# Kernel tuning notes

Measured on AMD Instinct MI355X. Metric: run time of the kernel, lower is better.

## Reference

```python
import jax, jax.numpy as jnp
import numpy as np

LN_EPS = 1e-5


def setup_inputs() -> dict:
    key = jax.random.key(0)
    k1, k2, k3 = jax.random.split(key, 3)
    N, E, D_IN, D_OUT = 50000, 500000, 128, 128
    x = jax.random.normal(k1, (N, D_IN), dtype=jnp.float32)
    edge_index = jax.random.randint(k2, (2, E), 0, N, dtype=jnp.int64)
    W = jax.random.normal(k3, (D_IN, D_OUT), dtype=jnp.float32) * (1.0 / np.sqrt(D_IN))
    b = jnp.zeros((D_OUT,), dtype=jnp.float32)
    ln_gamma = jnp.ones((D_OUT,), dtype=jnp.float32)
    ln_beta = jnp.zeros((D_OUT,), dtype=jnp.float32)
    return {"x": x, "edge_index": edge_index, "W": W, "b": b,
            "ln_gamma": ln_gamma, "ln_beta": ln_beta}


def reference(x, edge_index, W, b, ln_gamma, ln_beta):
    N = x.shape[0]
    # GCNConv: linear transform first (no fused bias; bias added after aggregation)
    h = x @ W  # [N, D_out]
    # add self-loops
    loops = jnp.arange(N, dtype=edge_index.dtype)
    src = jnp.concatenate([edge_index[0], loops])  # [E+N]
    dst = jnp.concatenate([edge_index[1], loops])  # [E+N]
    # symmetric normalization deg^{-1/2} (degree computed on dst, incl. self-loops)
    deg = jax.ops.segment_sum(jnp.ones(src.shape, dtype=h.dtype), dst, num_segments=N)
    dinv = jnp.where(deg > 0, jax.lax.rsqrt(deg), 0.0)
    norm = dinv[src] * dinv[dst]  # [E+N]
    # gather messages, scale, scatter-add to destinations
    msgs = h[src] * norm[:, None]  # [E+N, D_out]
    out = jax.ops.segment_sum(msgs, dst, num_segments=N) + b  # [N, D_out]
    # LayerNorm over features
    mu = out.mean(axis=-1, keepdims=True)
    var = out.var(axis=-1, keepdims=True)
    out = (out - mu) * jax.lax.rsqrt(var + LN_EPS) * ln_gamma + ln_beta
    # activation
    return jax.nn.relu(out)
```

## Files before the change

kernel.cpp:

```cpp
#include <hip/hip_runtime.h>
#include <math.h>

#define D 128
#define LN_EPS 1e-5f
#define BKT 64
#define DSTRIDE 32

__device__ __forceinline__ float bf_lo(unsigned u) {
    union { unsigned u; float f; } c; c.u = u << 16; return c.f;
}
__device__ __forceinline__ float bf_hi(unsigned u) {
    union { unsigned u; float f; } c; c.u = u & 0xffff0000u; return c.f;
}
__device__ __forceinline__ unsigned pack_bf2(float a, float b) {
    union { float f; unsigned u; } x, y; x.f = a; y.f = b;
    unsigned ua = x.u + (0x7fffu + ((x.u >> 16) & 1u));
    unsigned ub = y.u + (0x7fffu + ((y.u >> 16) & 1u));
    return (ua >> 16) | (ub & 0xffff0000u);
}

__global__ void gemm_kernel(const float* __restrict__ x, const float* __restrict__ W,
                            unsigned* __restrict__ h2, int N) {
    __shared__ float xs[64][D];
    int tid  = threadIdx.x;
    int row0 = blockIdx.x * 64;
#pragma unroll
    for (int i = 0; i < 8; ++i) {
        int idx = i * 256 + tid;
        int r   = idx >> 5;
        int c4  = idx & 31;
        float4 v = make_float4(0.f, 0.f, 0.f, 0.f);
        if (row0 + r < N) v = *(const float4*)&x[(size_t)(row0 + r) * D + c4 * 4];
        *(float4*)&xs[r][c4 * 4] = v;
    }
    __syncthreads();

    int cg    = tid & 31;
    int rbase = (tid >> 5) * 8;
    float4 acc[8];
#pragma unroll
    for (int i = 0; i < 8; ++i) acc[i] = make_float4(0.f, 0.f, 0.f, 0.f);

#pragma unroll 2
    for (int k = 0; k < D; k += 4) {
        float4 w0 = *(const float4*)&W[(k + 0) * D + cg * 4];
        float4 w1 = *(const float4*)&W[(k + 1) * D + cg * 4];
        float4 w2 = *(const float4*)&W[(k + 2) * D + cg * 4];
        float4 w3 = *(const float4*)&W[(k + 3) * D + cg * 4];
#pragma unroll
        for (int r = 0; r < 8; ++r) {
            float4 xv = *(const float4*)&xs[rbase + r][k];
            acc[r].x = fmaf(xv.x, w0.x, acc[r].x);
            acc[r].y = fmaf(xv.x, w0.y, acc[r].y);
            acc[r].z = fmaf(xv.x, w0.z, acc[r].z);
            acc[r].w = fmaf(xv.x, w0.w, acc[r].w);
            acc[r].x = fmaf(xv.y, w1.x, acc[r].x);
            acc[r].y = fmaf(xv.y, w1.y, acc[r].y);
            acc[r].z = fmaf(xv.y, w1.z, acc[r].z);
            acc[r].w = fmaf(xv.y, w1.w, acc[r].w);
            acc[r].x = fmaf(xv.z, w2.x, acc[r].x);
            acc[r].y = fmaf(xv.z, w2.y, acc[r].y);
            acc[r].z = fmaf(xv.z, w2.z, acc[r].z);
            acc[r].w = fmaf(xv.z, w2.w, acc[r].w);
            acc[r].x = fmaf(xv.w, w3.x, acc[r].x);
            acc[r].y = fmaf(xv.w, w3.y, acc[r].y);
            acc[r].z = fmaf(xv.w, w3.z, acc[r].z);
            acc[r].w = fmaf(xv.w, w3.w, acc[r].w);
        }
    }
#pragma unroll
    for (int r = 0; r < 8; ++r) {
        int row = row0 + rbase + r;
        if (row < N) {
            uint2 p = make_uint2(pack_bf2(acc[r].x, acc[r].y),
                                 pack_bf2(acc[r].z, acc[r].w));
            *(uint2*)&h2[(size_t)row * (D / 2) + cg * 2] = p;
        }
    }
}

__global__ void bucket_kernel(const int* __restrict__ src, const int* __restrict__ dst,
                              int* __restrict__ degp, int* __restrict__ bucket, int E) {
    int e = blockIdx.x * blockDim.x + threadIdx.x;
    if (e < E) {
        int d = dst[e];
        int p = atomicAdd(&degp[(size_t)d * DSTRIDE], 1);
        if (p < BKT) bucket[(size_t)d * BKT + p] = src[e];
    }
}

__global__ void finalize_kernel(const int* __restrict__ degp, int* __restrict__ degc,
                                float* __restrict__ dinv, int N) {
    int i = blockIdx.x * blockDim.x + threadIdx.x;
    if (i < N) {
        int d = degp[(size_t)i * DSTRIDE];
        degc[i] = d < BKT ? d : BKT;
        dinv[i] = rsqrtf((float)d + 1.0f);
    }
}

__global__ void gather_ln_kernel(const int* __restrict__ bucket, const int* __restrict__ degc,
                                 const float* __restrict__ dinv,
                                 const unsigned* __restrict__ h2, const float* __restrict__ b,
                                 const float* __restrict__ g, const float* __restrict__ be,
                                 float* __restrict__ out, int N) {
    int row  = blockIdx.x * 4 + (threadIdx.x >> 6);
    int lane = threadIdx.x & 63;
    if (row >= N) return;
    int dgc  = degc[row];
    float di = dinv[row];
    float sw = di * di;
    unsigned su = h2[(size_t)row * (D / 2) + lane];
    float acc0 = bf_lo(su) * sw;
    float acc1 = bf_hi(su) * sw;
    const int* bk = bucket + (size_t)row * BKT;
    int e = 0;
    for (; e + 3 < dgc; e += 4) {
        int s0 = bk[e], s1 = bk[e + 1], s2 = bk[e + 2], s3 = bk[e + 3];
        float w0 = dinv[s0] * di;
        float w1 = dinv[s1] * di;
        float w2 = dinv[s2] * di;
        float w3 = dinv[s3] * di;
        unsigned u0 = h2[(size_t)s0 * (D / 2) + lane];
        unsigned u1 = h2[(size_t)s1 * (D / 2) + lane];
        unsigned u2 = h2[(size_t)s2 * (D / 2) + lane];
        unsigned u3 = h2[(size_t)s3 * (D / 2) + lane];
        acc0 = fmaf(bf_lo(u0), w0, acc0);  acc1 = fmaf(bf_hi(u0), w0, acc1);
        acc0 = fmaf(bf_lo(u1), w1, acc0);  acc1 = fmaf(bf_hi(u1), w1, acc1);
        acc0 = fmaf(bf_lo(u2), w2, acc0);  acc1 = fmaf(bf_hi(u2), w2, acc1);
        acc0 = fmaf(bf_lo(u3), w3, acc0);  acc1 = fmaf(bf_hi(u3), w3, acc1);
    }
    for (; e < dgc; ++e) {
        int s = bk[e];
        float w = dinv[s] * di;
        unsigned u = h2[(size_t)s * (D / 2) + lane];
        acc0 = fmaf(bf_lo(u), w, acc0);
        acc1 = fmaf(bf_hi(u), w, acc1);
    }
    float2 bb = *(const float2*)&b[lane * 2];
    float v0 = acc0 + bb.x;
    float v1 = acc1 + bb.y;
    float s = v0 + v1;
    float q = v0 * v0 + v1 * v1;
#pragma unroll
    for (int off = 32; off; off >>= 1) {
        s += __shfl_xor(s, off);
        q += __shfl_xor(q, off);
    }
    float mean = s * (1.0f / 128.0f);
    float var  = q * (1.0f / 128.0f) - mean * mean;
    float rstd = rsqrtf(var + LN_EPS);
    float2 gg = *(const float2*)&g[lane * 2];
    float2 eb = *(const float2*)&be[lane * 2];
    float y0 = (v0 - mean) * rstd * gg.x + eb.x;
    float y1 = (v1 - mean) * rstd * gg.y + eb.y;
    *(float2*)&out[(size_t)row * D + lane * 2] = make_float2(fmaxf(y0, 0.0f), fmaxf(y1, 0.0f));
}

extern "C" void kernel_launch(void* const* d_in, const int* in_sizes, int n_in,
                              void* d_out, int out_size, void* d_ws, size_t ws_size,
                              hipStream_t stream) {
    const float* x  = (const float*)d_in[0];
    const int*   ei = (const int*)d_in[1];
    const float* W  = (const float*)d_in[2];
    const float* b  = (const float*)d_in[3];
    const float* g  = (const float*)d_in[4];
    const float* be = (const float*)d_in[5];

    int N = in_sizes[0] / D;
    int E = in_sizes[1] / 2;
    const int* src = ei;
    const int* dst = ei + E;

    float* out = (float*)d_out;

    char* w = (char*)d_ws;
    unsigned* h2   = (unsigned*)w;            w += (size_t)N * (D / 2) * sizeof(unsigned);
    int*   degp    = (int*)w;                 w += (size_t)N * DSTRIDE * sizeof(int);
    int*   degc    = (int*)w;                 w += (size_t)N * sizeof(int);
    float* dinv    = (float*)w;               w += (size_t)N * sizeof(float);
    int*   bucket  = (int*)w;                 w += (size_t)N * BKT * sizeof(int);

    hipMemsetAsync(degp, 0, (size_t)N * DSTRIDE * sizeof(int), stream);

    gemm_kernel    <<<(N + 63) / 64,   256, 0, stream>>>(x, W, h2, N);
    bucket_kernel  <<<(E + 255) / 256, 256, 0, stream>>>(src, dst, degp, bucket, E);
    finalize_kernel<<<(N + 255) / 256, 256, 0, stream>>>(degp, degc, dinv, N);
    gather_ln_kernel<<<(N + 3) / 4,    256, 0, stream>>>(bucket, degc, dinv, h2,
                                                         b, g, be, out, N);
}
```

Measured before the change: 171.2 us.

## Use fp16 MFMA for GEMM, compact degree array, deeper gather unroll

The GEMM switches from scalar FP32 FMAs to the 16x16x32 fp16 MFMA instruction. Both x and W are converted to fp16 in shared memory, and h is stored as packed fp16 rather than bf16. The degree counter array drops its 32-int padding stride, which shrinks the memset and the finalize reads but lets atomics on neighbouring nodes share cache lines. The gather loop is unrolled to 8 edges with the loads batched, to keep more memory requests in flight. Running the GEMM in fp16 and reloading W in every block could change accuracy and costs extra conversion work.

```diff
diff --git a/kernel.cpp b/kernel.cpp
--- a/kernel.cpp
+++ b/kernel.cpp
@@ -1,29 +1,21 @@
 #include <hip/hip_runtime.h>
+#include <hip/hip_fp16.h>
 #include <math.h>
 
 #define D 128
 #define LN_EPS 1e-5f
 #define BKT 64
-#define DSTRIDE 32
 
-__device__ __forceinline__ float bf_lo(unsigned u) {
-    union { unsigned u; float f; } c; c.u = u << 16; return c.f;
-}
-__device__ __forceinline__ float bf_hi(unsigned u) {
-    union { unsigned u; float f; } c; c.u = u & 0xffff0000u; return c.f;
-}
-__device__ __forceinline__ unsigned pack_bf2(float a, float b) {
-    union { float f; unsigned u; } x, y; x.f = a; y.f = b;
-    unsigned ua = x.u + (0x7fffu + ((x.u >> 16) & 1u));
-    unsigned ub = y.u + (0x7fffu + ((y.u >> 16) & 1u));
-    return (ua >> 16) | (ub & 0xffff0000u);
-}
+typedef _Float16 f16x8 __attribute__((ext_vector_type(8)));
+typedef float    f32x4 __attribute__((ext_vector_type(4)));
 
 __global__ void gemm_kernel(const float* __restrict__ x, const float* __restrict__ W,
                             unsigned* __restrict__ h2, int N) {
-    __shared__ float xs[64][D];
+    __shared__ _Float16 xs[64][136];
+    __shared__ _Float16 wt[128][136];
     int tid  = threadIdx.x;
     int row0 = blockIdx.x * 64;
+
 #pragma unroll
     for (int i = 0; i < 8; ++i) {
         int idx = i * 256 + tid;
@@ -31,72 +23,85 @@
         int c4  = idx & 31;
         float4 v = make_float4(0.f, 0.f, 0.f, 0.f);
         if (row0 + r < N) v = *(const float4*)&x[(size_t)(row0 + r) * D + c4 * 4];
-        *(float4*)&xs[r][c4 * 4] = v;
+        __half2 lo = __floats2half2_rn(v.x, v.y);
+        __half2 hi = __floats2half2_rn(v.z, v.w);
+        *(__half2*)&xs[r][c4 * 4]     = lo;
+        *(__half2*)&xs[r][c4 * 4 + 2] = hi;
+    }
+#pragma unroll
+    for (int i = 0; i < 16; ++i) {
+        int f  = i * 256 + tid;
+        int k  = f >> 5;
+        int n4 = f & 31;
+        float4 wv = *(const float4*)&W[k * D + n4 * 4];
+        wt[n4 * 4 + 0][k] = (_Float16)wv.x;
+        wt[n4 * 4 + 1][k] = (_Float16)wv.y;
+        wt[n4 * 4 + 2][k] = (_Float16)wv.z;
+        wt[n4 * 4 + 3][k] = (_Float16)wv.w;
     }
     __syncthreads();
 
-    int cg    = tid & 31;
-    int rbase = (tid >> 5) * 8;
-    float4 acc[8];
+    int l     = tid & 63;
+    int mtile = tid >> 6;
+    int mn    = l & 15;
+    int kq    = (l >> 4) * 8;
+    f32x4 acc[8];
 #pragma unroll
-    for (int i = 0; i < 8; ++i) acc[i] = make_float4(0.f, 0.f, 0.f, 0.f);
+    for (int nt = 0; nt < 8; ++nt) acc[nt] = (f32x4){0.f, 0.f, 0.f, 0.f};
 
-#pragma unroll 2
-    for (int k = 0; k < D; k += 4) {
-        float4 w0 = *(const float4*)&W[(k + 0) * D + cg * 4];
-        float4 w1 = *(const float4*)&W[(k + 1) * D + cg * 4];
-        float4 w2 = *(const float4*)&W[(k + 2) * D + cg * 4];
-        float4 w3 = *(const float4*)&W[(k + 3) * D + cg * 4];
 #pragma unroll
-        for (int r = 0; r < 8; ++r) {
-            float4 xv = *(const float4*)&xs[rbase + r][k];
-            acc[r].x = fmaf(xv.x, w0.x, acc[r].x);
-            acc[r].y = fmaf(xv.x, w0.y, acc[r].y);
-            acc[r].z = fmaf(xv.x, w0.z, acc[r].z);
-            acc[r].w = fmaf(xv.x, w0.w, acc[r].w);
-            acc[r].x = fmaf(xv.y, w1.x, acc[r].x);
-            acc[r].y = fmaf(xv.y, w1.y, acc[r].y);
-            acc[r].z = fmaf(xv.y, w1.z, acc[r].z);
-            acc[r].w = fmaf(xv.y, w1.w, acc[r].w);
-            acc[r].x = fmaf(xv.z, w2.x, acc[r].x);
-            acc[r].y = fmaf(xv.z, w2.y, acc[r].y);
-            acc[r].z = fmaf(xv.z, w2.z, acc[r].z);
-            acc[r].w = fmaf(xv.z, w2.w, acc[r].w);
-            acc[r].x = fmaf(xv.w, w3.x, acc[r].x);
-            acc[r].y = fmaf(xv.w, w3.y, acc[r].y);
-            acc[r].z = fmaf(xv.w, w3.z, acc[r].z);
-            acc[r].w = fmaf(xv.w, w3.w, acc[r].w);
+    for (int ks = 0; ks < 4; ++ks) {
+        int kb = ks * 32 + kq;
+        f16x8 a = *(f16x8*)&xs[mtile * 16 + mn][kb];
+#pragma unroll
+        for (int nt = 0; nt < 8; ++nt) {
+            f16x8 bf = *(f16x8*)&wt[nt * 16 + mn][kb];
+            acc[nt] = __builtin_amdgcn_mfma_f32_16x16x32_f16(a, bf, acc[nt], 0, 0, 0);
         }
     }
+
+    int quad = l >> 4;
 #pragma unroll
-    for (int r = 0; r < 8; ++r) {
-        int row = row0 + rbase + r;
-        if (row < N) {
-            uint2 p = make_uint2(pack_bf2(acc[r].x, acc[r].y),
-                                 pack_bf2(acc[r].z, acc[r].w));
-            *(uint2*)&h2[(size_t)row * (D / 2) + cg * 2] = p;
+    for (int nt = 0; nt < 8; ++nt) {
+#pragma unroll
+        for (int rg = 0; rg < 4; ++rg) {
+            float v  = acc[nt][rg];
+            float pv = __shfl_xor(v, 1);
+            if (!(l & 1)) {
+                int row = row0 + mtile * 16 + quad * 4 + rg;
+                if (row < N) {
+                    __half2 p = __floats2half2_rn(v, pv);
+                    h2[(size_t)row * (D / 2) + nt * 8 + (mn >> 1)] = *(unsigned*)&p;
+                }
+            }
         }
     }
 }
 
 __global__ void bucket_kernel(const int* __restrict__ src, const int* __restrict__ dst,
-                              int* __restrict__ degp, int* __restrict__ bucket, int E) {
+                              int* __restrict__ degi, int* __restrict__ bucket, int E) {
     int e = blockIdx.x * blockDim.x + threadIdx.x;
     if (e < E) {
         int d = dst[e];
-        int p = atomicAdd(&degp[(size_t)d * DSTRIDE], 1);
+        int p = atomicAdd(&degi[d], 1);
         if (p < BKT) bucket[(size_t)d * BKT + p] = src[e];
     }
 }
 
-__global__ void finalize_kernel(const int* __restrict__ degp, int* __restrict__ degc,
+__global__ void finalize_kernel(const int* __restrict__ degi, int* __restrict__ degc,
                                 float* __restrict__ dinv, int N) {
     int i = blockIdx.x * blockDim.x + threadIdx.x;
     if (i < N) {
-        int d = degp[(size_t)i * DSTRIDE];
+        int d = degi[i];
         degc[i] = d < BKT ? d : BKT;
         dinv[i] = rsqrtf((float)d + 1.0f);
     }
+}
+
+__device__ __forceinline__ void acc_edge(float& a0, float& a1, unsigned u, float w) {
+    __half2 hv = *(__half2*)&u;
+    a0 = fmaf(__low2float(hv),  w, a0);
+    a1 = fmaf(__high2float(hv), w, a1);
 }
 
 __global__ void gather_ln_kernel(const int* __restrict__ bucket, const int* __restrict__ degc,
@@ -111,31 +116,24 @@
     float di = dinv[row];
     float sw = di * di;
     unsigned su = h2[(size_t)row * (D / 2) + lane];
-    float acc0 = bf_lo(su) * sw;
-    float acc1 = bf_hi(su) * sw;
+    float acc0 = 0.f, acc1 = 0.f;
+    acc_edge(acc0, acc1, su, sw);
     const int* bk = bucket + (size_t)row * BKT;
     int e = 0;
-    for (; e + 3 < dgc; e += 4) {
-        int s0 = bk[e], s1 = bk[e + 1], s2 = bk[e + 2], s3 = bk[e + 3];
-        float w0 = dinv[s0] * di;
-        float w1 = dinv[s1] * di;
-        float w2 = dinv[s2] * di;
-        float w3 = dinv[s3] * di;
-        unsigned u0 = h2[(size_t)s0 * (D / 2) + lane];
-        unsigned u1 = h2[(size_t)s1 * (D / 2) + lane];
-        unsigned u2 = h2[(size_t)s2 * (D / 2) + lane];
-        unsigned u3 = h2[(size_t)s3 * (D / 2) + lane];
-        acc0 = fmaf(bf_lo(u0), w0, acc0);  acc1 = fmaf(bf_hi(u0), w0, acc1);
-        acc0 = fmaf(bf_lo(u1), w1, acc0);  acc1 = fmaf(bf_hi(u1), w1, acc1);
-        acc0 = fmaf(bf_lo(u2), w2, acc0);  acc1 = fmaf(bf_hi(u2), w2, acc1);
-        acc0 = fmaf(bf_lo(u3), w3, acc0);  acc1 = fmaf(bf_hi(u3), w3, acc1);
+    for (; e + 7 < dgc; e += 8) {
+        int   s[8]; float wgt[8]; unsigned u[8];
+#pragma unroll
+        for (int j = 0; j < 8; ++j) s[j] = bk[e + j];
+#pragma unroll
+        for (int j = 0; j < 8; ++j) wgt[j] = dinv[s[j]] * di;
+#pragma unroll
+        for (int j = 0; j < 8; ++j) u[j] = h2[(size_t)s[j] * (D / 2) + lane];
+#pragma unroll
+        for (int j = 0; j < 8; ++j) acc_edge(acc0, acc1, u[j], wgt[j]);
     }
     for (; e < dgc; ++e) {
         int s = bk[e];
-        float w = dinv[s] * di;
-        unsigned u = h2[(size_t)s * (D / 2) + lane];
-        acc0 = fmaf(bf_lo(u), w, acc0);
-        acc1 = fmaf(bf_hi(u), w, acc1);
+        acc_edge(acc0, acc1, h2[(size_t)s * (D / 2) + lane], dinv[s] * di);
     }
     float2 bb = *(const float2*)&b[lane * 2];
     float v0 = acc0 + bb.x;
@@ -176,16 +174,16 @@
 
     char* w = (char*)d_ws;
     unsigned* h2   = (unsigned*)w;            w += (size_t)N * (D / 2) * sizeof(unsigned);
-    int*   degp    = (int*)w;                 w += (size_t)N * DSTRIDE * sizeof(int);
+    int*   degi    = (int*)w;                 w += (size_t)N * sizeof(int);
     int*   degc    = (int*)w;                 w += (size_t)N * sizeof(int);
     float* dinv    = (float*)w;               w += (size_t)N * sizeof(float);
     int*   bucket  = (int*)w;                 w += (size_t)N * BKT * sizeof(int);
 
-    hipMemsetAsync(degp, 0, (size_t)N * DSTRIDE * sizeof(int), stream);
+    hipMemsetAsync(degi, 0, (size_t)N * sizeof(int), stream);
 
     gemm_kernel    <<<(N + 63) / 64,   256, 0, stream>>>(x, W, h2, N);
-    bucket_kernel  <<<(E + 255) / 256, 256, 0, stream>>>(src, dst, degp, bucket, E);
-    finalize_kernel<<<(N + 255) / 256, 256, 0, stream>>>(degp, degc, dinv, N);
+    bucket_kernel  <<<(E + 255) / 256, 256, 0, stream>>>(src, dst, degi, bucket, E);
+    finalize_kernel<<<(N + 255) / 256, 256, 0, stream>>>(degi, degc, dinv, N);
     gather_ln_kernel<<<(N + 3) / 4,    256, 0, stream>>>(bucket, degc, dinv, h2,
                                                          b, g, be, out, N);
 }
```

Result: no change. 171.8 us (+0.3%).
